# Kernel optimization log

Hardware: AMD Instinct MI355X
Metric: run time of the kernel (lower is better)

## Reference

```python
import jax, jax.numpy as jnp
import numpy as np

D_MODEL, D_HEAD, N_HEAD = 1024, 64, 16
B, S = 8, 1024


def setup_inputs() -> dict:
    key = jax.random.key(0)
    ks = jax.random.split(key, 11)
    sc = 1.0 / np.sqrt(D_MODEL)
    inp = {
        "query": jax.random.normal(ks[0], (B, S, D_MODEL), jnp.float32),
        "key": jax.random.normal(ks[1], (B, S, D_MODEL), jnp.float32),
        "value": jax.random.normal(ks[2], (B, S, D_MODEL), jnp.float32),
        # stacked per-head Q/K projections: [H, d_model, d_head]
        "Wq": jax.random.normal(ks[3], (N_HEAD, D_MODEL, D_HEAD), jnp.float32) * sc,
        "bq": jax.random.normal(ks[4], (N_HEAD, D_HEAD), jnp.float32) * 0.01,
        "Wk": jax.random.normal(ks[5], (N_HEAD, D_MODEL, D_HEAD), jnp.float32) * sc,
        "bk": jax.random.normal(ks[6], (N_HEAD, D_HEAD), jnp.float32) * 0.01,
        # shared V projection
        "Wv": jax.random.normal(ks[7], (D_MODEL, D_HEAD), jnp.float32) * sc,
        "bv": jax.random.normal(ks[8], (D_HEAD,), jnp.float32) * 0.01,
        # output projection d_head -> d_model
        "Wo": jax.random.normal(ks[9], (D_HEAD, D_MODEL), jnp.float32) * (1.0 / np.sqrt(D_HEAD)),
        "bo": jax.random.normal(ks[10], (D_MODEL,), jnp.float32) * 0.01,
    }
    return inp


def reference(query, key, value, Wq, bq, Wk, bk, Wv, bv, Wo, bo):
    scale = D_HEAD ** -0.5
    # per-head projections, batched over heads: [B, H, S, d_head]
    Q = jnp.einsum("bsd,hdk->bhsk", query, Wq) + bq[None, :, None, :]
    K = jnp.einsum("bsd,hdk->bhsk", key, Wk) + bk[None, :, None, :]
    # shared V: [B, S, d_head]
    V = value @ Wv + bv
    # attention weights per head: [B, H, S, S]
    wei = jax.nn.softmax(jnp.einsum("bhsk,bhtk->bhst", Q, K) * scale, axis=-1)
    # head outputs averaged (shared V): [B, S, d_head]
    out = jnp.mean(jnp.einsum("bhst,btk->bhsk", wei, V), axis=1)
    return out @ Wo + bo
```

## Files before the change

### kernel.cpp

```cpp
#include <hip/hip_runtime.h>
#include <hip/hip_bf16.h>
#include <math.h>

typedef __attribute__((ext_vector_type(4))) float  f32x4;
typedef __attribute__((ext_vector_type(8))) __bf16 bf16x8;
typedef __attribute__((ext_vector_type(4))) __bf16 bf16x4;
typedef __attribute__((ext_vector_type(4))) short  s16x4;

#define SCL 0.18033688011111543f
#define MFMA16(a, b, c)   __builtin_amdgcn_mfma_f32_16x16x32_bf16((a), (b), (c), 0, 0, 0)
#define MFMA16K16(a, b, c) __builtin_amdgcn_mfma_f32_16x16x16bf16_1k((a), (b), (c), 0, 0, 0)

union B4 { bf16x4 b; s16x4 s; };

__global__ __launch_bounds__(256) void pack_qk(
    const float* __restrict__ Wq, const float* __restrict__ Wk,
    __bf16* __restrict__ WqT, __bf16* __restrict__ WkT)
{
    __shared__ __bf16 T0[64][68];
    __shared__ __bf16 T1[64][68];
    const int tid = threadIdx.x;
    const int h = blockIdx.x & 15, kt = blockIdx.x >> 4;
    const int kk = tid >> 2, cf = (tid & 3) * 16;
    const size_t base = (size_t)h * 65536 + (size_t)(kt * 64 + kk) * 64 + cf;
    #pragma unroll
    for (int j = 0; j < 4; ++j) {
        f32x4 v = *(const f32x4*)&Wq[base + 4 * j];
        f32x4 u = *(const f32x4*)&Wk[base + 4 * j];
        bf16x4 vb, ub;
        #pragma unroll
        for (int e = 0; e < 4; ++e) { vb[e] = (__bf16)v[e]; ub[e] = (__bf16)u[e]; }
        *(bf16x4*)&T0[kk][cf + 4 * j] = vb;
        *(bf16x4*)&T1[kk][cf + 4 * j] = ub;
    }
    __syncthreads();
    const int c = tid >> 2, k8 = (tid & 3) * 16;
    bf16x8 q0, q1, k0v, k1v;
    #pragma unroll
    for (int j = 0; j < 8; ++j) {
        q0[j] = T0[k8 + j][c];     q1[j] = T0[k8 + 8 + j][c];
        k0v[j] = T1[k8 + j][c];    k1v[j] = T1[k8 + 8 + j][c];
    }
    size_t dst = (size_t)(h * 64 + c) * 1024 + kt * 64 + k8;
    *(bf16x8*)&WqT[dst] = q0;  *(bf16x8*)&WqT[dst + 8] = q1;
    *(bf16x8*)&WkT[dst] = k0v; *(bf16x8*)&WkT[dst + 8] = k1v;
}

__global__ __launch_bounds__(256) void pack_misc(
    const float* __restrict__ Wv, const float* __restrict__ bv,
    const float* __restrict__ Wo,
    __bf16* __restrict__ WvT, float* __restrict__ bvP, __bf16* __restrict__ WoT)
{
    int idx = blockIdx.x * 256 + threadIdx.x;
    if (idx < 131072) {
        int n = idx >> 10, k = idx & 1023;
        WvT[idx] = (n < 64) ? (__bf16)Wv[k * 64 + n] : (__bf16)0.0f;
    }
    if (idx < 65536) {
        int n = idx >> 6, d = idx & 63;
        WoT[idx] = (__bf16)Wo[d * 1024 + n];
    }
    if (idx < 128) bvP[idx] = (idx < 64) ? bv[idx] : 0.0f;
}

__global__ __launch_bounds__(256, 2) void proj_gemm_f32(
    const float* __restrict__ A, const __bf16* __restrict__ Bt,
    const float* __restrict__ bias, __bf16* __restrict__ C, float oscale)
{
    __shared__ __bf16 As[2][128][72];
    __shared__ __bf16 Bs[2][128][72];

    const int tid = threadIdx.x;
    const int lane = tid & 63, w = tid >> 6;
    const int wr = w >> 1, wc = w & 1;
    const int l15 = lane & 15, g = lane >> 4;
    const int m0 = blockIdx.x * 128, n0 = blockIdx.y * 128;
    const int arow = tid >> 4, acf = (tid & 15) * 4;
    const int brow = tid >> 3, bc8 = (tid & 7) * 8;

    f32x4 areg[8];
    bf16x8 breg[4];
    #pragma unroll
    for (int p = 0; p < 8; ++p)
        areg[p] = *(const f32x4*)&A[(size_t)(m0 + arow + 16 * p) * 1024 + acf];
    #pragma unroll
    for (int p = 0; p < 4; ++p)
        breg[p] = *(const bf16x8*)&Bt[(size_t)(n0 + brow + 32 * p) * 1024 + bc8];

    f32x4 acc[4][4] = {};
    int cur = 0;
    for (int k0 = 0; k0 < 1024; k0 += 64) {
        #pragma unroll
        for (int p = 0; p < 8; ++p) {
            bf16x4 c4;
            #pragma unroll
            for (int e = 0; e < 4; ++e) c4[e] = (__bf16)areg[p][e];
            *(bf16x4*)&As[cur][arow + 16 * p][acf] = c4;
        }
        #pragma unroll
        for (int p = 0; p < 4; ++p)
            *(bf16x8*)&Bs[cur][brow + 32 * p][bc8] = breg[p];
        if (k0 < 960) {
            #pragma unroll
            for (int p = 0; p < 8; ++p)
                areg[p] = *(const f32x4*)&A[(size_t)(m0 + arow + 16 * p) * 1024 + k0 + 64 + acf];
            #pragma unroll
            for (int p = 0; p < 4; ++p)
                breg[p] = *(const bf16x8*)&Bt[(size_t)(n0 + brow + 32 * p) * 1024 + k0 + 64 + bc8];
        }
        __syncthreads();
        __builtin_amdgcn_s_setprio(1);
        #pragma unroll
        for (int ks = 0; ks < 2; ++ks) {
            bf16x8 af[4], bfv[4];
            #pragma unroll
            for (int mi = 0; mi < 4; ++mi)
                af[mi] = *(const bf16x8*)&As[cur][64 * wr + 16 * mi + l15][32 * ks + 8 * g];
            #pragma unroll
            for (int ni = 0; ni < 4; ++ni)
                bfv[ni] = *(const bf16x8*)&Bs[cur][64 * wc + 16 * ni + l15][32 * ks + 8 * g];
            #pragma unroll
            for (int mi = 0; mi < 4; ++mi)
                #pragma unroll
                for (int ni = 0; ni < 4; ++ni)
                    acc[mi][ni] = MFMA16(af[mi], bfv[ni], acc[mi][ni]);
        }
        __builtin_amdgcn_s_setprio(0);
        cur ^= 1;
    }

    #pragma unroll
    for (int mi = 0; mi < 4; ++mi)
        #pragma unroll
        for (int ni = 0; ni < 4; ++ni) {
            int n = n0 + 64 * wc + 16 * ni + l15;
            float bn = bias[n];
            #pragma unroll
            for (int r = 0; r < 4; ++r) {
                int m = m0 + 64 * wr + 16 * mi + 4 * g + r;
                C[(size_t)m * 1024 + n] = (__bf16)((acc[mi][ni][r] + bn) * oscale);
            }
        }
}

__global__ __launch_bounds__(256, 2) void proj_v(
    const float* __restrict__ A, const __bf16* __restrict__ Bt,
    const float* __restrict__ bias, __bf16* __restrict__ C)
{
    __shared__ __bf16 As[2][64][72];
    __shared__ __bf16 Bs[2][64][72];

    const int tid = threadIdx.x;
    const int lane = tid & 63, w = tid >> 6;
    const int wr = w >> 1, wc = w & 1;
    const int l15 = lane & 15, g = lane >> 4;
    const int m0 = blockIdx.x * 64;
    const int arow = tid >> 2, acf = (tid & 3) * 16;
    const int bcf = (tid & 3) * 16;

    f32x4 areg[4];
    bf16x8 breg[2];
    #pragma unroll
    for (int j = 0; j < 4; ++j)
        areg[j] = *(const f32x4*)&A[(size_t)(m0 + arow) * 1024 + acf + 4 * j];
    #pragma unroll
    for (int j = 0; j < 2; ++j)
        breg[j] = *(const bf16x8*)&Bt[(size_t)arow * 1024 + bcf + 8 * j];

    f32x4 acc[2][2] = {};
    int cur = 0;
    for (int k0 = 0; k0 < 1024; k0 += 64) {
        #pragma unroll
        for (int j = 0; j < 4; ++j) {
            bf16x4 c4;
            #pragma unroll
            for (int e = 0; e < 4; ++e) c4[e] = (__bf16)areg[j][e];
            *(bf16x4*)&As[cur][arow][acf + 4 * j] = c4;
        }
        #pragma unroll
        for (int j = 0; j < 2; ++j)
            *(bf16x8*)&Bs[cur][arow][bcf + 8 * j] = breg[j];
        if (k0 < 960) {
            #pragma unroll
            for (int j = 0; j < 4; ++j)
                areg[j] = *(const f32x4*)&A[(size_t)(m0 + arow) * 1024 + k0 + 64 + acf + 4 * j];
            #pragma unroll
            for (int j = 0; j < 2; ++j)
                breg[j] = *(const bf16x8*)&Bt[(size_t)arow * 1024 + k0 + 64 + bcf + 8 * j];
        }
        __syncthreads();
        #pragma unroll
        for (int ks = 0; ks < 2; ++ks) {
            bf16x8 af[2], bfv[2];
            #pragma unroll
            for (int mi = 0; mi < 2; ++mi)
                af[mi] = *(const bf16x8*)&As[cur][32 * wr + 16 * mi + l15][32 * ks + 8 * g];
            #pragma unroll
            for (int ni = 0; ni < 2; ++ni)
                bfv[ni] = *(const bf16x8*)&Bs[cur][32 * wc + 16 * ni + l15][32 * ks + 8 * g];
            #pragma unroll
            for (int mi = 0; mi < 2; ++mi)
                #pragma unroll
                for (int ni = 0; ni < 2; ++ni)
                    acc[mi][ni] = MFMA16(af[mi], bfv[ni], acc[mi][ni]);
        }
        __syncthreads();
        cur ^= 1;
    }

    #pragma unroll
    for (int mi = 0; mi < 2; ++mi)
        #pragma unroll
        for (int ni = 0; ni < 2; ++ni) {
            int n = 32 * wc + 16 * ni + l15;
            float bn = bias[n];
            #pragma unroll
            for (int r = 0; r < 4; ++r) {
                int m = m0 + 32 * wr + 16 * mi + 4 * g + r;
                C[(size_t)n * 8192 + m] = (__bf16)(acc[mi][ni][r] + bn);
            }
        }
}

__global__ __launch_bounds__(128, 4) void attn_kernel(
    const __bf16* __restrict__ Qb, const __bf16* __restrict__ Kb,
    const __bf16* __restrict__ Vt, __bf16* __restrict__ Oh)
{
    __shared__ __bf16 Ks[2][32][72];
    __shared__ __bf16 Vs[2][64][44];

    const int qt = blockIdx.x, bh = blockIdx.y;
    const int b = bh >> 4, h = bh & 15;
    const int tid = threadIdx.x;
    const int lane = tid & 63, w = tid >> 6;
    const int l15 = lane & 15, g = lane >> 4;
    const int s0 = b * 1024 + qt * 64;

    const int krow = tid >> 2, kc = (tid & 3) * 16;
    const int vrow = tid >> 1, vc = (tid & 1) * 16;

    bf16x8 qf[2][2];
    #pragma unroll
    for (int mi = 0; mi < 2; ++mi)
        #pragma unroll
        for (int ks = 0; ks < 2; ++ks)
            qf[mi][ks] = *(const bf16x8*)
                &Qb[(size_t)(s0 + 32 * w + 16 * mi + l15) * 1024 + h * 64 + 32 * ks + 8 * g];

    const __bf16* Kbase = Kb + (size_t)(b * 1024) * 1024 + h * 64;
    const __bf16* Vbase = Vt + (size_t)b * 1024;

    bf16x8 kreg[2], vreg[2];
    #pragma unroll
    for (int j = 0; j < 2; ++j) {
        kreg[j] = *(const bf16x8*)&Kbase[(size_t)krow * 1024 + kc + 8 * j];
        vreg[j] = *(const bf16x8*)&Vbase[(size_t)vrow * 8192 + vc + 8 * j];
    }

    f32x4 acc_o[2][4] = {};
    float l_par[2] = {0.0f, 0.0f};

    int cur = 0;
    for (int it = 0; it < 32; ++it) {
        *(bf16x8*)&Ks[cur][krow][kc]     = kreg[0];
        *(bf16x8*)&Ks[cur][krow][kc + 8] = kreg[1];
        *(bf16x8*)&Vs[cur][vrow][vc]     = vreg[0];
        *(bf16x8*)&Vs[cur][vrow][vc + 8] = vreg[1];
        if (it < 31) {
            int t1 = (it + 1) * 32;
            #pragma unroll
            for (int j = 0; j < 2; ++j) {
                kreg[j] = *(const bf16x8*)&Kbase[(size_t)(t1 + krow) * 1024 + kc + 8 * j];
                vreg[j] = *(const bf16x8*)&Vbase[(size_t)vrow * 8192 + t1 + vc + 8 * j];
            }
        }
        __syncthreads();

        f32x4 pacc[2][2] = {};
        __builtin_amdgcn_s_setprio(1);
        #pragma unroll
        for (int ks = 0; ks < 2; ++ks) {
            bf16x8 kf[2];
            #pragma unroll
            for (int ni = 0; ni < 2; ++ni)
                kf[ni] = *(const bf16x8*)&Ks[cur][16 * ni + l15][32 * ks + 8 * g];
            #pragma unroll
            for (int mi = 0; mi < 2; ++mi)
                #pragma unroll
                for (int ni = 0; ni < 2; ++ni)
                    pacc[mi][ni] = MFMA16(kf[ni], qf[mi][ks], pacc[mi][ni]);
        }
        __builtin_amdgcn_s_setprio(0);

        s16x4 pb[2][2];
        #pragma unroll
        for (int mi = 0; mi < 2; ++mi) {
            float rs = 0.0f;
            #pragma unroll
            for (int ni = 0; ni < 2; ++ni) {
                B4 pk;
                #pragma unroll
                for (int r = 0; r < 4; ++r) {
                    float pv = exp2f(pacc[mi][ni][r]);
                    rs += pv;
                    pk.b[r] = (__bf16)pv;
                }
                pb[mi][ni] = pk.s;
            }
            l_par[mi] += rs;
        }

        __builtin_amdgcn_s_setprio(1);
        #pragma unroll
        for (int c = 0; c < 2; ++c) {
            s16x4 vf[4];
            #pragma unroll
            for (int nd = 0; nd < 4; ++nd) {
                B4 vv;
                vv.b = *(const bf16x4*)&Vs[cur][16 * nd + l15][16 * c + 4 * g];
                vf[nd] = vv.s;
            }
            #pragma unroll
            for (int mi = 0; mi < 2; ++mi)
                #pragma unroll
                for (int nd = 0; nd < 4; ++nd)
                    acc_o[mi][nd] = MFMA16K16(vf[nd], pb[mi][c], acc_o[mi][nd]);
        }
        __builtin_amdgcn_s_setprio(0);
        cur ^= 1;
    }

    #pragma unroll
    for (int mi = 0; mi < 2; ++mi) {
        float l = l_par[mi];
        l += __shfl_xor(l, 16);
        l += __shfl_xor(l, 32);
        float rl = 1.0f / l;
        int q = qt * 64 + 32 * w + 16 * mi + l15;
        #pragma unroll
        for (int nd = 0; nd < 4; ++nd) {
            bf16x4 ov;
            #pragma unroll
            for (int r = 0; r < 4; ++r) ov[r] = (__bf16)(acc_o[mi][nd][r] * rl);
            *(bf16x4*)&Oh[(size_t)(bh * 1024 + q) * 64 + 16 * nd + 4 * g] = ov;
        }
    }
}

__global__ __launch_bounds__(256) void mean_kernel(
    const __bf16* __restrict__ Oh, __bf16* __restrict__ Om)
{
    int idx = blockIdx.x * 256 + threadIdx.x;
    int m = idx >> 3, d8 = (idx & 7) * 8;
    int b = m >> 10, q = m & 1023;
    const __bf16* src = Oh + (size_t)(b * 16) * 65536 + (size_t)q * 64 + d8;
    float s[8] = {};
    #pragma unroll
    for (int h = 0; h < 16; ++h) {
        bf16x8 v = *(const bf16x8*)&src[(size_t)h * 65536];
        #pragma unroll
        for (int j = 0; j < 8; ++j) s[j] += (float)v[j];
    }
    bf16x8 o;
    #pragma unroll
    for (int j = 0; j < 8; ++j) o[j] = (__bf16)(s[j] * 0.0625f);
    *(bf16x8*)&Om[(size_t)m * 64 + d8] = o;
}

__global__ __launch_bounds__(256, 4) void out_gemm(
    const __bf16* __restrict__ Om, const __bf16* __restrict__ WoT,
    const float* __restrict__ bo, float* __restrict__ out)
{
    const int tid = threadIdx.x;
    const int lane = tid & 63, w = tid >> 6;
    const int wr = w >> 1, wc = w & 1;
    const int l15 = lane & 15, g = lane >> 4;
    const int m0 = blockIdx.x * 128, n0 = blockIdx.y * 128;

    f32x4 acc[4][4] = {};
    #pragma unroll
    for (int ks = 0; ks < 2; ++ks) {
        bf16x8 af[4], bfv[4];
        #pragma unroll
        for (int mi = 0; mi < 4; ++mi)
            af[mi] = *(const bf16x8*)&Om[(size_t)(m0 + 64 * wr + 16 * mi + l15) * 64 + 32 * ks + 8 * g];
        #pragma unroll
        for (int ni = 0; ni < 4; ++ni)
            bfv[ni] = *(const bf16x8*)&WoT[(size_t)(n0 + 64 * wc + 16 * ni + l15) * 64 + 32 * ks + 8 * g];
        #pragma unroll
        for (int mi = 0; mi < 4; ++mi)
            #pragma unroll
            for (int ni = 0; ni < 4; ++ni)
                acc[mi][ni] = MFMA16(af[mi], bfv[ni], acc[mi][ni]);
    }
    #pragma unroll
    for (int mi = 0; mi < 4; ++mi)
        #pragma unroll
        for (int ni = 0; ni < 4; ++ni) {
            int n = n0 + 64 * wc + 16 * ni + l15;
            float bn = bo[n];
            #pragma unroll
            for (int r = 0; r < 4; ++r) {
                int m = m0 + 64 * wr + 16 * mi + 4 * g + r;
                out[(size_t)m * 1024 + n] = acc[mi][ni][r] + bn;
            }
        }
}

extern "C" void kernel_launch(void* const* d_in, const int* in_sizes, int n_in,
                              void* d_out, int out_size, void* d_ws, size_t ws_size,
                              hipStream_t stream)
{
    const float* query = (const float*)d_in[0];
    const float* key_  = (const float*)d_in[1];
    const float* value = (const float*)d_in[2];
    const float* Wq = (const float*)d_in[3];
    const float* bq = (const float*)d_in[4];
    const float* Wk = (const float*)d_in[5];
    const float* bk = (const float*)d_in[6];
    const float* Wv = (const float*)d_in[7];
    const float* bv = (const float*)d_in[8];
    const float* Wo = (const float*)d_in[9];
    const float* bo = (const float*)d_in[10];
    float* out = (float*)d_out;

    char* p = (char*)d_ws;
    __bf16* Qbuf = (__bf16*)p; p += 8192ull * 1024 * 2;
    __bf16* Kbuf = (__bf16*)p; p += 8192ull * 1024 * 2;
    __bf16* VtB  = (__bf16*)p; p += 64ull * 8192 * 2;
    __bf16* WqT  = (__bf16*)p; p += 1024ull * 1024 * 2;
    __bf16* WkT  = (__bf16*)p; p += 1024ull * 1024 * 2;
    __bf16* WvT  = (__bf16*)p; p += 128ull * 1024 * 2;
    __bf16* WoT  = (__bf16*)p; p += 1024ull * 64 * 2;
    float*  bvP  = (float*)p;  p += 128 * 4;
    __bf16* Oh   = (__bf16*)p; p += 8ull * 16 * 1024 * 64 * 2;
    __bf16* Om   = (__bf16*)p; p += 8192ull * 64 * 2;

    pack_qk<<<256, 256, 0, stream>>>(Wq, Wk, WqT, WkT);
    pack_misc<<<512, 256, 0, stream>>>(Wv, bv, Wo, WvT, bvP, WoT);
    proj_gemm_f32<<<dim3(64, 8), 256, 0, stream>>>(query, WqT, bq, Qbuf, SCL);
    proj_gemm_f32<<<dim3(64, 8), 256, 0, stream>>>(key_,  WkT, bk, Kbuf, 1.0f);
    proj_v<<<128, 256, 0, stream>>>(value, WvT, bvP, VtB);
    attn_kernel<<<dim3(16, 128), 128, 0, stream>>>(Qbuf, Kbuf, VtB, Oh);
    mean_kernel<<<256, 256, 0, stream>>>(Oh, Om);
    out_gemm<<<dim3(64, 8), 256, 0, stream>>>(Om, WoT, bo, out);
}
```

Measured before the change: 156.6 us.

## Retile Q/K projection GEMM, load V fragments directly to registers, fast exp2

The Q/K projection GEMM moves to 128x256 output tiles with a K-step of 32, so each block reads the fp32 activations once per 256 output columns and the grid shrinks to half the blocks, at the cost of more accumulator registers. The attention kernel drops the V shared-memory staging and loads MFMA V fragments straight from global memory into double-buffered registers, which removes LDS traffic and raises occupancy to 5 blocks per SM. Softmax exponentials use a raw v_exp_f32 instruction in place of exp2f. The per-lane V loads are narrow bf16x4 reads, which may coalesce poorly.

```diff
diff --git a/kernel.cpp b/kernel.cpp
--- a/kernel.cpp
+++ b/kernel.cpp
@@ -12,6 +12,12 @@
 #define MFMA16K16(a, b, c) __builtin_amdgcn_mfma_f32_16x16x16bf16_1k((a), (b), (c), 0, 0, 0)
 
 union B4 { bf16x4 b; s16x4 s; };
+
+__device__ __forceinline__ float exp2_fast(float x) {
+    float r;
+    asm("v_exp_f32 %0, %1" : "=v"(r) : "v"(x));
+    return r;
+}
 
 __global__ __launch_bounds__(256) void pack_qk(
     const float* __restrict__ Wq, const float* __restrict__ Wk,
@@ -67,63 +73,60 @@
     const float* __restrict__ A, const __bf16* __restrict__ Bt,
     const float* __restrict__ bias, __bf16* __restrict__ C, float oscale)
 {
-    __shared__ __bf16 As[2][128][72];
-    __shared__ __bf16 Bs[2][128][72];
+    __shared__ __bf16 As[2][128][36];
+    __shared__ __bf16 Bs[2][256][36];
 
     const int tid = threadIdx.x;
     const int lane = tid & 63, w = tid >> 6;
     const int wr = w >> 1, wc = w & 1;
     const int l15 = lane & 15, g = lane >> 4;
-    const int m0 = blockIdx.x * 128, n0 = blockIdx.y * 128;
-    const int arow = tid >> 4, acf = (tid & 15) * 4;
-    const int brow = tid >> 3, bc8 = (tid & 7) * 8;
-
-    f32x4 areg[8];
+    const int m0 = blockIdx.x * 128, n0 = blockIdx.y * 256;
+    const int arow = tid >> 1, acf = (tid & 1) * 16;
+    const int brow = tid;
+
+    f32x4 areg[4];
     bf16x8 breg[4];
     #pragma unroll
-    for (int p = 0; p < 8; ++p)
-        areg[p] = *(const f32x4*)&A[(size_t)(m0 + arow + 16 * p) * 1024 + acf];
-    #pragma unroll
-    for (int p = 0; p < 4; ++p)
-        breg[p] = *(const bf16x8*)&Bt[(size_t)(n0 + brow + 32 * p) * 1024 + bc8];
-
-    f32x4 acc[4][4] = {};
+    for (int j = 0; j < 4; ++j) {
+        areg[j] = *(const f32x4*)&A[(size_t)(m0 + arow) * 1024 + acf + 4 * j];
+        breg[j] = *(const bf16x8*)&Bt[(size_t)(n0 + brow) * 1024 + 8 * j];
+    }
+
+    f32x4 acc[4][8] = {};
     int cur = 0;
-    for (int k0 = 0; k0 < 1024; k0 += 64) {
-        #pragma unroll
-        for (int p = 0; p < 8; ++p) {
+    for (int k0 = 0; k0 < 1024; k0 += 32) {
+        #pragma unroll
+        for (int j = 0; j < 4; ++j) {
             bf16x4 c4;
             #pragma unroll
-            for (int e = 0; e < 4; ++e) c4[e] = (__bf16)areg[p][e];
-            *(bf16x4*)&As[cur][arow + 16 * p][acf] = c4;
-        }
-        #pragma unroll
-        for (int p = 0; p < 4; ++p)
-            *(bf16x8*)&Bs[cur][brow + 32 * p][bc8] = breg[p];
-        if (k0 < 960) {
-            #pragma unroll
-            for (int p = 0; p < 8; ++p)
-                areg[p] = *(const f32x4*)&A[(size_t)(m0 + arow + 16 * p) * 1024 + k0 + 64 + acf];
-            #pragma unroll
-            for (int p = 0; p < 4; ++p)
-                breg[p] = *(const bf16x8*)&Bt[(size_t)(n0 + brow + 32 * p) * 1024 + k0 + 64 + bc8];
+            for (int e = 0; e < 4; ++e) c4[e] = (__bf16)areg[j][e];
+            *(bf16x4*)&As[cur][arow][acf + 4 * j] = c4;
+            *(bf16x8*)&Bs[cur][brow][8 * j] = breg[j];
+        }
+        if (k0 < 992) {
+            #pragma unroll
+            for (int j = 0; j < 4; ++j) {
+                areg[j] = *(const f32x4*)&A[(size_t)(m0 + arow) * 1024 + k0 + 32 + acf + 4 * j];
+                breg[j] = *(const bf16x8*)&Bt[(size_t)(n0 + brow) * 1024 + k0 + 32 + 8 * j];
+            }
         }
         __syncthreads();
         __builtin_amdgcn_s_setprio(1);
-        #pragma unroll
-        for (int ks = 0; ks < 2; ++ks) {
-            bf16x8 af[4], bfv[4];
+        bf16x8 af[4];
+        #pragma unroll
+        for (int mi = 0; mi < 4; ++mi)
+            af[mi] = *(const bf16x8*)&As[cur][64 * wr + 16 * mi + l15][8 * g];
+        #pragma unroll
+        for (int nh = 0; nh < 2; ++nh) {
+            bf16x8 bfv[4];
+            #pragma unroll
+            for (int nj = 0; nj < 4; ++nj)
+                bfv[nj] = *(const bf16x8*)&Bs[cur][128 * wc + 16 * (4 * nh + nj) + l15][8 * g];
             #pragma unroll
             for (int mi = 0; mi < 4; ++mi)
-                af[mi] = *(const bf16x8*)&As[cur][64 * wr + 16 * mi + l15][32 * ks + 8 * g];
-            #pragma unroll
-            for (int ni = 0; ni < 4; ++ni)
-                bfv[ni] = *(const bf16x8*)&Bs[cur][64 * wc + 16 * ni + l15][32 * ks + 8 * g];
-            #pragma unroll
-            for (int mi = 0; mi < 4; ++mi)
-                #pragma unroll
-                for (int ni = 0; ni < 4; ++ni)
-                    acc[mi][ni] = MFMA16(af[mi], bfv[ni], acc[mi][ni]);
+                #pragma unroll
+                for (int nj = 0; nj < 4; ++nj)
+                    acc[mi][4 * nh + nj] = MFMA16(af[mi], bfv[nj], acc[mi][4 * nh + nj]);
         }
         __builtin_amdgcn_s_setprio(0);
         cur ^= 1;
@@ -132,8 +135,8 @@
     #pragma unroll
     for (int mi = 0; mi < 4; ++mi)
         #pragma unroll
-        for (int ni = 0; ni < 4; ++ni) {
-            int n = n0 + 64 * wc + 16 * ni + l15;
+        for (int ni = 0; ni < 8; ++ni) {
+            int n = n0 + 128 * wc + 16 * ni + l15;
             float bn = bias[n];
             #pragma unroll
             for (int r = 0; r < 4; ++r) {
@@ -222,12 +225,11 @@
         }
 }
 
-__global__ __launch_bounds__(128, 4) void attn_kernel(
+__global__ __launch_bounds__(128, 5) void attn_kernel(
     const __bf16* __restrict__ Qb, const __bf16* __restrict__ Kb,
     const __bf16* __restrict__ Vt, __bf16* __restrict__ Oh)
 {
     __shared__ __bf16 Ks[2][32][72];
-    __shared__ __bf16 Vs[2][64][44];
 
     const int qt = blockIdx.x, bh = blockIdx.y;
     const int b = bh >> 4, h = bh & 15;
@@ -237,7 +239,6 @@
     const int s0 = b * 1024 + qt * 64;
 
     const int krow = tid >> 2, kc = (tid & 3) * 16;
-    const int vrow = tid >> 1, vc = (tid & 1) * 16;
 
     bf16x8 qf[2][2];
     #pragma unroll
@@ -248,31 +249,37 @@
                 &Qb[(size_t)(s0 + 32 * w + 16 * mi + l15) * 1024 + h * 64 + 32 * ks + 8 * g];
 
     const __bf16* Kbase = Kb + (size_t)(b * 1024) * 1024 + h * 64;
-    const __bf16* Vbase = Vt + (size_t)b * 1024;
-
-    bf16x8 kreg[2], vreg[2];
-    #pragma unroll
-    for (int j = 0; j < 2; ++j) {
+    const __bf16* Vrow  = Vt + (size_t)l15 * 8192 + b * 1024 + 4 * g;
+
+    bf16x8 kreg[2];
+    #pragma unroll
+    for (int j = 0; j < 2; ++j)
         kreg[j] = *(const bf16x8*)&Kbase[(size_t)krow * 1024 + kc + 8 * j];
-        vreg[j] = *(const bf16x8*)&Vbase[(size_t)vrow * 8192 + vc + 8 * j];
-    }
+
+    bf16x4 vfA[2][4], vfB[2][4];
+    #pragma unroll
+    for (int c = 0; c < 2; ++c)
+        #pragma unroll
+        for (int nd = 0; nd < 4; ++nd)
+            vfA[c][nd] = *(const bf16x4*)&Vrow[(size_t)nd * 131072 + 16 * c];
 
     f32x4 acc_o[2][4] = {};
     float l_par[2] = {0.0f, 0.0f};
-
     int cur = 0;
-    for (int it = 0; it < 32; ++it) {
+
+    auto step = [&](bf16x4 (&vcur)[2][4], bf16x4 (&vnext)[2][4], int it) {
         *(bf16x8*)&Ks[cur][krow][kc]     = kreg[0];
         *(bf16x8*)&Ks[cur][krow][kc + 8] = kreg[1];
-        *(bf16x8*)&Vs[cur][vrow][vc]     = vreg[0];
-        *(bf16x8*)&Vs[cur][vrow][vc + 8] = vreg[1];
-        if (it < 31) {
+        if (it + 1 < 32) {
             int t1 = (it + 1) * 32;
             #pragma unroll
-            for (int j = 0; j < 2; ++j) {
+            for (int j = 0; j < 2; ++j)
                 kreg[j] = *(const bf16x8*)&Kbase[(size_t)(t1 + krow) * 1024 + kc + 8 * j];
-                vreg[j] = *(const bf16x8*)&Vbase[(size_t)vrow * 8192 + t1 + vc + 8 * j];
-            }
+            #pragma unroll
+            for (int c = 0; c < 2; ++c)
+                #pragma unroll
+                for (int nd = 0; nd < 4; ++nd)
+                    vnext[c][nd] = *(const bf16x4*)&Vrow[(size_t)nd * 131072 + t1 + 16 * c];
         }
         __syncthreads();
 
@@ -301,7 +308,7 @@
                 B4 pk;
                 #pragma unroll
                 for (int r = 0; r < 4; ++r) {
-                    float pv = exp2f(pacc[mi][ni][r]);
+                    float pv = exp2_fast(pacc[mi][ni][r]);
                     rs += pv;
                     pk.b[r] = (__bf16)pv;
                 }
@@ -312,22 +319,21 @@
 
         __builtin_amdgcn_s_setprio(1);
         #pragma unroll
-        for (int c = 0; c < 2; ++c) {
-            s16x4 vf[4];
+        for (int c = 0; c < 2; ++c)
             #pragma unroll
             for (int nd = 0; nd < 4; ++nd) {
-                B4 vv;
-                vv.b = *(const bf16x4*)&Vs[cur][16 * nd + l15][16 * c + 4 * g];
-                vf[nd] = vv.s;
-            }
-            #pragma unroll
-            for (int mi = 0; mi < 2; ++mi)
-                #pragma unroll
-                for (int nd = 0; nd < 4; ++nd)
-                    acc_o[mi][nd] = MFMA16K16(vf[nd], pb[mi][c], acc_o[mi][nd]);
-        }
+                B4 vv; vv.b = vcur[c][nd];
+                #pragma unroll
+                for (int mi = 0; mi < 2; ++mi)
+                    acc_o[mi][nd] = MFMA16K16(vv.s, pb[mi][c], acc_o[mi][nd]);
+            }
         __builtin_amdgcn_s_setprio(0);
         cur ^= 1;
+    };
+
+    for (int it = 0; it < 32; it += 2) {
+        step(vfA, vfB, it);
+        step(vfB, vfA, it + 1);
     }
 
     #pragma unroll
@@ -438,8 +444,8 @@
 
     pack_qk<<<256, 256, 0, stream>>>(Wq, Wk, WqT, WkT);
     pack_misc<<<512, 256, 0, stream>>>(Wv, bv, Wo, WvT, bvP, WoT);
-    proj_gemm_f32<<<dim3(64, 8), 256, 0, stream>>>(query, WqT, bq, Qbuf, SCL);
-    proj_gemm_f32<<<dim3(64, 8), 256, 0, stream>>>(key_,  WkT, bk, Kbuf, 1.0f);
+    proj_gemm_f32<<<dim3(64, 4), 256, 0, stream>>>(query, WqT, bq, Qbuf, SCL);
+    proj_gemm_f32<<<dim3(64, 4), 256, 0, stream>>>(key_,  WkT, bk, Kbuf, 1.0f);
     proj_v<<<128, 256, 0, stream>>>(value, WvT, bvP, VtB);
     attn_kernel<<<dim3(16, 128), 128, 0, stream>>>(Qbuf, Kbuf, VtB, Oh);
     mean_kernel<<<256, 256, 0, stream>>>(Oh, Om);
```

Measured after the change: 378.7 us. +141.8%, slower.

## Retile projection GEMM to 128x256 with 512 threads, use raw v_exp in attention

Applied to the files above, without the earlier changes.

The Q/K projection GEMM moves to 512-thread blocks with 128x256 output tiles and a K-step of 32. Each block loads the fp32 activation tile once for twice as many output columns, which halves how often A is re-read across the N dimension, at the cost of smaller K stages and more barriers per tile. The attention softmax now calls the raw v_exp_f32 instruction through inline asm instead of exp2f, dropping range and denormal handling. The padding of the K shared-memory tile also changes from 72 to 68 columns.

```diff
diff --git a/kernel.cpp b/kernel.cpp
--- a/kernel.cpp
+++ b/kernel.cpp
@@ -12,6 +12,12 @@
 #define MFMA16K16(a, b, c) __builtin_amdgcn_mfma_f32_16x16x16bf16_1k((a), (b), (c), 0, 0, 0)
 
 union B4 { bf16x4 b; s16x4 s; };
+
+__device__ __forceinline__ float exp2_fast(float x) {
+    float r;
+    asm("v_exp_f32 %0, %1" : "=v"(r) : "v"(x));
+    return r;
+}
 
 __global__ __launch_bounds__(256) void pack_qk(
     const float* __restrict__ Wq, const float* __restrict__ Wk,
@@ -63,68 +69,61 @@
     if (idx < 128) bvP[idx] = (idx < 64) ? bv[idx] : 0.0f;
 }
 
-__global__ __launch_bounds__(256, 2) void proj_gemm_f32(
+__global__ __launch_bounds__(512, 2) void proj_gemm_f32(
     const float* __restrict__ A, const __bf16* __restrict__ Bt,
     const float* __restrict__ bias, __bf16* __restrict__ C, float oscale)
 {
-    __shared__ __bf16 As[2][128][72];
-    __shared__ __bf16 Bs[2][128][72];
+    __shared__ __bf16 As[2][128][36];
+    __shared__ __bf16 Bs[2][256][36];
 
     const int tid = threadIdx.x;
     const int lane = tid & 63, w = tid >> 6;
-    const int wr = w >> 1, wc = w & 1;
+    const int wr = w >> 2, wc = w & 3;
     const int l15 = lane & 15, g = lane >> 4;
-    const int m0 = blockIdx.x * 128, n0 = blockIdx.y * 128;
-    const int arow = tid >> 4, acf = (tid & 15) * 4;
-    const int brow = tid >> 3, bc8 = (tid & 7) * 8;
-
-    f32x4 areg[8];
-    bf16x8 breg[4];
-    #pragma unroll
-    for (int p = 0; p < 8; ++p)
-        areg[p] = *(const f32x4*)&A[(size_t)(m0 + arow + 16 * p) * 1024 + acf];
-    #pragma unroll
-    for (int p = 0; p < 4; ++p)
-        breg[p] = *(const bf16x8*)&Bt[(size_t)(n0 + brow + 32 * p) * 1024 + bc8];
+    const int m0 = blockIdx.x * 128, n0 = blockIdx.y * 256;
+    const int arow = tid >> 2, acf = (tid & 3) * 8;
+    const int brow = tid >> 1, bcf = (tid & 1) * 16;
+
+    f32x4 areg[2];
+    bf16x8 breg[2];
+    #pragma unroll
+    for (int j = 0; j < 2; ++j) {
+        areg[j] = *(const f32x4*)&A[(size_t)(m0 + arow) * 1024 + acf + 4 * j];
+        breg[j] = *(const bf16x8*)&Bt[(size_t)(n0 + brow) * 1024 + bcf + 8 * j];
+    }
 
     f32x4 acc[4][4] = {};
     int cur = 0;
-    for (int k0 = 0; k0 < 1024; k0 += 64) {
-        #pragma unroll
-        for (int p = 0; p < 8; ++p) {
+    for (int k0 = 0; k0 < 1024; k0 += 32) {
+        #pragma unroll
+        for (int j = 0; j < 2; ++j) {
             bf16x4 c4;
             #pragma unroll
-            for (int e = 0; e < 4; ++e) c4[e] = (__bf16)areg[p][e];
-            *(bf16x4*)&As[cur][arow + 16 * p][acf] = c4;
-        }
-        #pragma unroll
-        for (int p = 0; p < 4; ++p)
-            *(bf16x8*)&Bs[cur][brow + 32 * p][bc8] = breg[p];
-        if (k0 < 960) {
-            #pragma unroll
-            for (int p = 0; p < 8; ++p)
-                areg[p] = *(const f32x4*)&A[(size_t)(m0 + arow + 16 * p) * 1024 + k0 + 64 + acf];
-            #pragma unroll
-            for (int p = 0; p < 4; ++p)
-                breg[p] = *(const bf16x8*)&Bt[(size_t)(n0 + brow + 32 * p) * 1024 + k0 + 64 + bc8];
+            for (int e = 0; e < 4; ++e) c4[e] = (__bf16)areg[j][e];
+            *(bf16x4*)&As[cur][arow][acf + 4 * j] = c4;
+            *(bf16x8*)&Bs[cur][brow][bcf + 8 * j] = breg[j];
+        }
+        if (k0 < 992) {
+            #pragma unroll
+            for (int j = 0; j < 2; ++j) {
+                areg[j] = *(const f32x4*)&A[(size_t)(m0 + arow) * 1024 + k0 + 32 + acf + 4 * j];
+                breg[j] = *(const bf16x8*)&Bt[(size_t)(n0 + brow) * 1024 + k0 + 32 + bcf + 8 * j];
+            }
         }
         __syncthreads();
         __builtin_amdgcn_s_setprio(1);
-        #pragma unroll
-        for (int ks = 0; ks < 2; ++ks) {
-            bf16x8 af[4], bfv[4];
-            #pragma unroll
-            for (int mi = 0; mi < 4; ++mi)
-                af[mi] = *(const bf16x8*)&As[cur][64 * wr + 16 * mi + l15][32 * ks + 8 * g];
+        bf16x8 af[4], bfv[4];
+        #pragma unroll
+        for (int mi = 0; mi < 4; ++mi)
+            af[mi] = *(const bf16x8*)&As[cur][64 * wr + 16 * mi + l15][8 * g];
+        #pragma unroll
+        for (int ni = 0; ni < 4; ++ni)
+            bfv[ni] = *(const bf16x8*)&Bs[cur][64 * wc + 16 * ni + l15][8 * g];
+        #pragma unroll
+        for (int mi = 0; mi < 4; ++mi)
             #pragma unroll
             for (int ni = 0; ni < 4; ++ni)
-                bfv[ni] = *(const bf16x8*)&Bs[cur][64 * wc + 16 * ni + l15][32 * ks + 8 * g];
-            #pragma unroll
-            for (int mi = 0; mi < 4; ++mi)
-                #pragma unroll
-                for (int ni = 0; ni < 4; ++ni)
-                    acc[mi][ni] = MFMA16(af[mi], bfv[ni], acc[mi][ni]);
-        }
+                acc[mi][ni] = MFMA16(af[mi], bfv[ni], acc[mi][ni]);
         __builtin_amdgcn_s_setprio(0);
         cur ^= 1;
     }
@@ -226,7 +225,7 @@
     const __bf16* __restrict__ Qb, const __bf16* __restrict__ Kb,
     const __bf16* __restrict__ Vt, __bf16* __restrict__ Oh)
 {
-    __shared__ __bf16 Ks[2][32][72];
+    __shared__ __bf16 Ks[2][32][68];
     __shared__ __bf16 Vs[2][64][44];
 
     const int qt = blockIdx.x, bh = blockIdx.y;
@@ -301,7 +300,7 @@
                 B4 pk;
                 #pragma unroll
                 for (int r = 0; r < 4; ++r) {
-                    float pv = exp2f(pacc[mi][ni][r]);
+                    float pv = exp2_fast(pacc[mi][ni][r]);
                     rs += pv;
                     pk.b[r] = (__bf16)pv;
                 }
@@ -438,8 +437,8 @@
 
     pack_qk<<<256, 256, 0, stream>>>(Wq, Wk, WqT, WkT);
     pack_misc<<<512, 256, 0, stream>>>(Wv, bv, Wo, WvT, bvP, WoT);
-    proj_gemm_f32<<<dim3(64, 8), 256, 0, stream>>>(query, WqT, bq, Qbuf, SCL);
-    proj_gemm_f32<<<dim3(64, 8), 256, 0, stream>>>(key_,  WkT, bk, Kbuf, 1.0f);
+    proj_gemm_f32<<<dim3(64, 4), 512, 0, stream>>>(query, WqT, bq, Qbuf, SCL);
+    proj_gemm_f32<<<dim3(64, 4), 512, 0, stream>>>(key_,  WkT, bk, Kbuf, 1.0f);
     proj_v<<<128, 256, 0, stream>>>(value, WvT, bvP, VtB);
     attn_kernel<<<dim3(16, 128), 128, 0, stream>>>(Qbuf, Kbuf, VtB, Oh);
     mean_kernel<<<256, 256, 0, stream>>>(Oh, Om);
```

Result: faster. 143.7 us (-8.2%).

## Merge pack and Q/K projection launches, use raw v_exp, retune K tile padding

Applied to the files above, without the earlier changes.

Folds the two weight-packing kernels into one launch and runs the Q and K projection GEMMs as a single grid with a z dimension that picks operands. This removes two kernel launches and lets the Q and K GEMM blocks share one wave of scheduling. In the attention softmax, exp2f is replaced with an inline v_exp_f32 instruction to avoid the library's range handling. The K shared-memory row padding also changes from 72 to 68, which may change LDS bank-conflict behaviour.

```diff
diff --git a/kernel.cpp b/kernel.cpp
--- a/kernel.cpp
+++ b/kernel.cpp
@@ -13,13 +13,35 @@
 
 union B4 { bf16x4 b; s16x4 s; };
 
-__global__ __launch_bounds__(256) void pack_qk(
+__device__ __forceinline__ float exp2_fast(float x) {
+    float r;
+    asm("v_exp_f32 %0, %1" : "=v"(r) : "v"(x));
+    return r;
+}
+
+__global__ __launch_bounds__(256) void pack_all(
     const float* __restrict__ Wq, const float* __restrict__ Wk,
-    __bf16* __restrict__ WqT, __bf16* __restrict__ WkT)
-{
+    const float* __restrict__ Wv, const float* __restrict__ bv,
+    const float* __restrict__ Wo,
+    __bf16* __restrict__ WqT, __bf16* __restrict__ WkT,
+    __bf16* __restrict__ WvT, float* __restrict__ bvP, __bf16* __restrict__ WoT)
+{
+    const int tid = threadIdx.x;
+    if (blockIdx.x >= 256) {
+        int idx = (blockIdx.x - 256) * 256 + tid;
+        if (idx < 131072) {
+            int n = idx >> 10, k = idx & 1023;
+            WvT[idx] = (n < 64) ? (__bf16)Wv[k * 64 + n] : (__bf16)0.0f;
+        }
+        if (idx < 65536) {
+            int n = idx >> 6, d = idx & 63;
+            WoT[idx] = (__bf16)Wo[d * 1024 + n];
+        }
+        if (idx < 128) bvP[idx] = (idx < 64) ? bv[idx] : 0.0f;
+        return;
+    }
     __shared__ __bf16 T0[64][68];
     __shared__ __bf16 T1[64][68];
-    const int tid = threadIdx.x;
     const int h = blockIdx.x & 15, kt = blockIdx.x >> 4;
     const int kk = tid >> 2, cf = (tid & 3) * 16;
     const size_t base = (size_t)h * 65536 + (size_t)(kt * 64 + kk) * 64 + cf;
@@ -46,27 +68,19 @@
     *(bf16x8*)&WkT[dst] = k0v; *(bf16x8*)&WkT[dst + 8] = k1v;
 }
 
-__global__ __launch_bounds__(256) void pack_misc(
-    const float* __restrict__ Wv, const float* __restrict__ bv,
-    const float* __restrict__ Wo,
-    __bf16* __restrict__ WvT, float* __restrict__ bvP, __bf16* __restrict__ WoT)
-{
-    int idx = blockIdx.x * 256 + threadIdx.x;
-    if (idx < 131072) {
-        int n = idx >> 10, k = idx & 1023;
-        WvT[idx] = (n < 64) ? (__bf16)Wv[k * 64 + n] : (__bf16)0.0f;
-    }
-    if (idx < 65536) {
-        int n = idx >> 6, d = idx & 63;
-        WoT[idx] = (__bf16)Wo[d * 1024 + n];
-    }
-    if (idx < 128) bvP[idx] = (idx < 64) ? bv[idx] : 0.0f;
-}
-
-__global__ __launch_bounds__(256, 2) void proj_gemm_f32(
-    const float* __restrict__ A, const __bf16* __restrict__ Bt,
-    const float* __restrict__ bias, __bf16* __restrict__ C, float oscale)
-{
+__global__ __launch_bounds__(256, 2) void proj_qk(
+    const float* __restrict__ Aq, const float* __restrict__ Ak,
+    const __bf16* __restrict__ WqT, const __bf16* __restrict__ WkT,
+    const float* __restrict__ bq, const float* __restrict__ bk,
+    __bf16* __restrict__ Cq, __bf16* __restrict__ Ck)
+{
+    const int z = blockIdx.z;
+    const float* A  = z ? Ak : Aq;
+    const __bf16* Bt = z ? WkT : WqT;
+    const float* bias = z ? bk : bq;
+    __bf16* C = z ? Ck : Cq;
+    const float oscale = z ? 1.0f : SCL;
+
     __shared__ __bf16 As[2][128][72];
     __shared__ __bf16 Bs[2][128][72];
 
@@ -226,7 +240,7 @@
     const __bf16* __restrict__ Qb, const __bf16* __restrict__ Kb,
     const __bf16* __restrict__ Vt, __bf16* __restrict__ Oh)
 {
-    __shared__ __bf16 Ks[2][32][72];
+    __shared__ __bf16 Ks[2][32][68];
     __shared__ __bf16 Vs[2][64][44];
 
     const int qt = blockIdx.x, bh = blockIdx.y;
@@ -301,7 +315,7 @@
                 B4 pk;
                 #pragma unroll
                 for (int r = 0; r < 4; ++r) {
-                    float pv = exp2f(pacc[mi][ni][r]);
+                    float pv = exp2_fast(pacc[mi][ni][r]);
                     rs += pv;
                     pk.b[r] = (__bf16)pv;
                 }
@@ -436,10 +450,8 @@
     __bf16* Oh   = (__bf16*)p; p += 8ull * 16 * 1024 * 64 * 2;
     __bf16* Om   = (__bf16*)p; p += 8192ull * 64 * 2;
 
-    pack_qk<<<256, 256, 0, stream>>>(Wq, Wk, WqT, WkT);
-    pack_misc<<<512, 256, 0, stream>>>(Wv, bv, Wo, WvT, bvP, WoT);
-    proj_gemm_f32<<<dim3(64, 8), 256, 0, stream>>>(query, WqT, bq, Qbuf, SCL);
-    proj_gemm_f32<<<dim3(64, 8), 256, 0, stream>>>(key_,  WkT, bk, Kbuf, 1.0f);
+    pack_all<<<768, 256, 0, stream>>>(Wq, Wk, Wv, bv, Wo, WqT, WkT, WvT, bvP, WoT);
+    proj_qk<<<dim3(64, 8, 2), 256, 0, stream>>>(query, key_, WqT, WkT, bq, bk, Qbuf, Kbuf);
     proj_v<<<128, 256, 0, stream>>>(value, WvT, bvP, VtB);
     attn_kernel<<<dim3(16, 128), 128, 0, stream>>>(Qbuf, Kbuf, VtB, Oh);
     mean_kernel<<<256, 256, 0, stream>>>(Oh, Om);
```

New measurement: 140.5 us, median of 4. -10.3%, faster.
